# Kernel tuning notes

Hardware: AMD Instinct MI355X
Metric: run time of the kernel (lower is better)

The kernel has to match this reference:

```python
import jax, jax.numpy as jnp
import numpy as np

N = 3072          # num nodes
H = 256           # hidden_features
B = 4             # num_heads
HD = H // B       # per-head dim
PRIOR_MU = 1.0
PRIOR_SIGMA = 1.0
LN_EPS = 1e-5


def setup_inputs() -> dict:
    key = jax.random.key(0)
    ks = jax.random.split(key, 12)
    s = 0.02  # weight init scale
    return {
        "h": jax.random.normal(ks[0], (N, H), jnp.float32),
        "gamma": jnp.ones((H,), jnp.float32),
        "beta": jnp.zeros((H,), jnp.float32),
        "W_k": jax.random.normal(ks[1], (H, H), jnp.float32) * s,
        "b_k": jnp.zeros((H,), jnp.float32),
        "W_mu": jax.random.normal(ks[2], (H, H), jnp.float32) * s,
        "b_mu": jnp.zeros((H,), jnp.float32),
        "W_ls": jax.random.normal(ks[3], (H, H), jnp.float32) * s,
        "b_ls": jnp.zeros((H,), jnp.float32),
        "W_v": jax.random.normal(ks[4], (H * B, H), jnp.float32) * s,
        "b_v": jnp.zeros((H,), jnp.float32),
        "diffusion": jax.random.uniform(ks[5], (N, N, 1), jnp.float32),
        "eps": jax.random.normal(ks[6], (N, N, B), jnp.float32),
    }


def reference(h, gamma, beta, W_k, b_k, W_mu, b_mu, W_ls, b_ls, W_v, b_v, diffusion, eps):
    h0 = h
    # LayerNorm
    mean = jnp.mean(h, axis=-1, keepdims=True)
    var = jnp.var(h, axis=-1, keepdims=True)
    hn = (h - mean) * jax.lax.rsqrt(var + LN_EPS) * gamma + beta
    # Q/K-style projections, split into heads: [N, HD, B]
    k = (hn @ W_k + b_k).reshape(N, HD, B)
    mu = (hn @ W_mu + b_mu).reshape(N, HD, B)
    ls = (hn @ W_ls + b_ls).reshape(N, HD, B)
    scale = HD ** -0.5
    mu = jnp.einsum('xyb,zyb->xzb', k, mu) * scale       # [N, N, B]
    ls = jnp.einsum('xyb,zyb->xzb', k, ls) * scale       # [N, N, B]
    sigma = jax.nn.softplus(ls)
    # KL(LogNormal(mu, sigma) || LogNormal(log(prior_mu), prior_sigma))
    mu_p = jnp.log(jnp.asarray(PRIOR_MU, h.dtype))
    sig_p = jnp.asarray(PRIOR_SIGMA, h.dtype)
    kl = (jnp.log(sig_p / sigma)
          + (sigma ** 2 + (mu - mu_p) ** 2) / (2.0 * sig_p ** 2)
          - 0.5)
    kl = (kl * jnp.sign(diffusion)).sum(-1).mean()
    # reparameterized LogNormal sample, masked by diffusion matrix
    a = jnp.exp(mu + sigma * eps) * diffusion            # [N, N, B]
    # L1 normalize over source-node axis (dim=-2), torch F.normalize semantics
    denom = jnp.clip(jnp.sum(jnp.abs(a), axis=-2, keepdims=True), 1e-12)
    a = a / denom
    # diffusion-weighted aggregation: [N, B, H] -> [N, B*H]
    out = jnp.einsum('xyb,yz->xbz', a, hn).reshape(N, B * H)
    out = out @ W_v + b_v                                 # fc_v (dropout = eval mode)
    out = jax.nn.elu(out) + h0
    return out, kl
```

## Files before the change

### kernel.cpp

```cpp
#include <hip/hip_runtime.h>
#include <hip/hip_bf16.h>


#define NN 3072
#define HH 256
#define NB 4
#define HD 64
constexpr int KMLSZ = 192 * 2 * 64 * 8;

typedef __attribute__((ext_vector_type(8))) short bf16x8;
typedef __attribute__((ext_vector_type(4))) float f32x4;

static __device__ inline short f2bf(float f) {
    __hip_bfloat16 h = __float2bfloat16(f);
    return __builtin_bit_cast(short, h);
}

typedef const __attribute__((address_space(1))) unsigned int* gas_ptr;
typedef __attribute__((address_space(3))) unsigned int* las_ptr;
static __device__ inline void gload_lds16(const void* g, void* l) {
    __builtin_amdgcn_global_load_lds((gas_ptr)g, (las_ptr)l, 16, 0, 0);
}

__global__ void k0_prep(const float* __restrict__ Wk, const float* __restrict__ Wmu,
                        const float* __restrict__ Wls, const float* __restrict__ bk,
                        const float* __restrict__ bmu, const float* __restrict__ bls,
                        const float* __restrict__ Wv, short* __restrict__ WTcat,
                        float* __restrict__ biascat, short* __restrict__ WvT,
                        float* __restrict__ denom) {
    __shared__ float t[64][65];
    int bx = blockIdx.x;
    if (bx < 48) {
        int mat = bx >> 4;
        int by = (bx >> 2) & 3, bc = bx & 3;
        int y0 = by * 64, c0 = bc * 64;
        const float* W = (mat == 0) ? Wk : (mat == 1 ? Wmu : Wls);
        float scale = (mat == 0) ? 0.125f : 1.f;
        int r = threadIdx.x >> 4, c4 = (threadIdx.x & 15) * 4;
#pragma unroll
        for (int i = 0; i < 4; i++) {
            int yl = r + i * 16;
            float4 v = *(const float4*)(W + (y0 + yl) * 256 + c0 + c4);
            t[yl][c4] = v.x; t[yl][c4 + 1] = v.y; t[yl][c4 + 2] = v.z; t[yl][c4 + 3] = v.w;
        }
        __syncthreads();
#pragma unroll
        for (int i = 0; i < 4; i++) {
            int cl = r + i * 16;
            int corig = c0 + cl;
            int cp = mat * 256 + (corig & 3) * 64 + (corig >> 2);
            short4 v = make_short4(f2bf(t[c4][cl] * scale), f2bf(t[c4 + 1][cl] * scale),
                                   f2bf(t[c4 + 2][cl] * scale), f2bf(t[c4 + 3][cl] * scale));
            *(short4*)(WTcat + cp * 256 + y0 + c4) = v;
        }
        return;
    }
    if (bx < 112) {
        int b = bx - 48;
        int bk2 = b >> 2, bn = b & 3;
        int k0 = bk2 * 64, n0 = bn * 64;
        int r = threadIdx.x >> 4, c4 = (threadIdx.x & 15) * 4;
#pragma unroll
        for (int i = 0; i < 4; i++) {
            int kk = r + i * 16;
            float4 v = *(const float4*)(Wv + (k0 + kk) * 256 + n0 + c4);
            t[kk][c4] = v.x; t[kk][c4 + 1] = v.y; t[kk][c4 + 2] = v.z; t[kk][c4 + 3] = v.w;
        }
        __syncthreads();
#pragma unroll
        for (int i = 0; i < 4; i++) {
            int nn = r + i * 16;
            short4 v = make_short4(f2bf(t[c4][nn]), f2bf(t[c4 + 1][nn]),
                                   f2bf(t[c4 + 2][nn]), f2bf(t[c4 + 3][nn]));
            *(short4*)(WvT + (n0 + nn) * 1024 + k0 + c4) = v;
        }
        return;
    }
    if (bx == 112) {
        int cc = threadIdx.x;
        int corig = (cc & 63) * 4 + (cc >> 6);
        biascat[cc] = bk[corig] * 0.125f;
        biascat[256 + cc] = bmu[corig];
        biascat[512 + cc] = bls[corig];
        return;
    }
    int i = (bx - 113) * 256 + threadIdx.x;
    if (i < 13312) denom[i] = 0.f;
}

__global__ void k1_ln(const float* __restrict__ h, const float* __restrict__ gamma,
                      const float* __restrict__ beta, short* __restrict__ hn) {
    int row = blockIdx.x, tid = threadIdx.x;
    float v = h[row * 256 + tid];
    float s = v, s2 = v * v;
    for (int off = 32; off; off >>= 1) {
        s += __shfl_xor(s, off);
        s2 += __shfl_xor(s2, off);
    }
    __shared__ float red[8];
    int w = tid >> 6, lane = tid & 63;
    if (!lane) { red[w] = s; red[4 + w] = s2; }
    __syncthreads();
    s = red[0] + red[1] + red[2] + red[3];
    s2 = red[4] + red[5] + red[6] + red[7];
    float mean = s * (1.f / 256.f);
    float var = s2 * (1.f / 256.f) - mean * mean;
    float rs = rsqrtf(var + 1e-5f);
    hn[row * 256 + tid] = f2bf((v - mean) * rs * gamma[tid] + beta[tid]);
}

__global__ void k1b_tr(const short* __restrict__ hn, short* __restrict__ hnT) {
    __shared__ short t[64][68];
    int bn = blockIdx.x >> 2, bh = blockIdx.x & 3;
    int n0 = bn * 64, h0 = bh * 64;
    int r = threadIdx.x >> 4, c4 = (threadIdx.x & 15) * 4;
#pragma unroll
    for (int i = 0; i < 4; i++) {
        int nn = r + i * 16;
        *(short4*)&t[nn][c4] = *(const short4*)(hn + (n0 + nn) * 256 + h0 + c4);
    }
    __syncthreads();
#pragma unroll
    for (int i = 0; i < 4; i++) {
        int hh = r + i * 16;
        short4 v = make_short4(t[c4][hh], t[c4 + 1][hh], t[c4 + 2][hh], t[c4 + 3][hh]);
        *(short4*)(hnT + (h0 + hh) * NN + n0 + c4) = v;
    }
}

__global__ __launch_bounds__(256) void k2_proj(const short* __restrict__ hn,
                                               const short* __restrict__ WTcat,
                                               const float* __restrict__ biascat,
                                               short* __restrict__ kml) {
    int bx = blockIdx.x;
    int mt = bx / 12, nb = bx % 12;
    int m0 = mt * 64, n0 = nb * 64;
    int tid = threadIdx.x, w = tid >> 6, lane = tid & 63, q = lane >> 4, c = lane & 15;
    int mrow = m0 + w * 16;
    f32x4 acc[4] = {{0, 0, 0, 0}, {0, 0, 0, 0}, {0, 0, 0, 0}, {0, 0, 0, 0}};
    for (int k0 = 0; k0 < 256; k0 += 32) {
        bf16x8 af = *(const bf16x8*)(hn + (mrow + c) * 256 + k0 + q * 8);
#pragma unroll
        for (int nt = 0; nt < 4; nt++) {
            bf16x8 bf = *(const bf16x8*)(WTcat + (n0 + nt * 16 + c) * 256 + k0 + q * 8);
            acc[nt] = __builtin_amdgcn_mfma_f32_16x16x32_bf16(af, bf, acc[nt], 0, 0, 0);
        }
    }
#pragma unroll
    for (int nt = 0; nt < 4; nt++) {
        int cp = n0 + nt * 16 + c;
        float bias = biascat[cp];
        int mat = cp >> 8, b = (cp >> 6) & 3, y = cp & 63;
        short* dst = kml + (size_t)(mat * 4 + b) * KMLSZ;
        int kh2 = y >> 5, lq = (y >> 3) & 3, j = y & 7;
        int zt = mt * 4 + w;
#pragma unroll
        for (int r = 0; r < 4; r++) {
            int ml = 4 * q + r;
            dst[(((zt * 2 + kh2) * 64) + lq * 16 + ml) * 8 + j] = f2bf(acc[nt][r] + bias);
        }
    }
}

__global__ __launch_bounds__(256) void k3a_elem(
    const short* __restrict__ kml, const float* __restrict__ eps,
    const float* __restrict__ diff, short* __restrict__ apk,
    float* __restrict__ denom, float* __restrict__ klsum) {
    __shared__ short frag[2][16][512];
    __shared__ float klred[4];
    const int tid = threadIdx.x;
    const int w = tid >> 6, lane = tid & 63, q = lane >> 4, c = lane & 15;
    const int xb = blockIdx.x % 48;
    const int zc = blockIdx.x / 48;
    const int xt = xb * 4 + w;
    const int x0 = xt * 16;

    auto stage = [&](int buf, int zt2) {
#pragma unroll
        for (int i = 0; i < 4; i++) {
            int f = w * 4 + i;
            int mat = f >> 3, bh = (f >> 1) & 3, kh = f & 1;
            const short* plane = kml + (size_t)((mat + 1) * 4 + bh) * KMLSZ;
            gload_lds16(plane + ((zt2 * 2 + kh) * 64 + lane) * 8, &frag[buf][f][0]);
        }
    };

    bf16x8 qf[NB][2];
#pragma unroll
    for (int b = 0; b < NB; b++)
#pragma unroll
        for (int kh = 0; kh < 2; kh++)
            qf[b][kh] = *(const bf16x8*)(kml + (size_t)b * KMLSZ +
                                         ((xt * 2 + kh) * 64 + lane) * 8);

    stage(0, zc * 4);

    float den_acc[NB] = {0.f, 0.f, 0.f, 0.f};
    float kl_acc = 0.f;
    const size_t xrow = (size_t)(x0 + c) * NN;

    for (int t = 0; t < 4; t++) {
        const int buf = t & 1;
        const int zt2 = zc * 4 + t;
        const int z16 = zt2 * 16;
        __syncthreads();
        if (t < 3) stage(buf ^ 1, zt2 + 1);
        f32x4 e4[4];
        float dif[4];
#pragma unroll
        for (int r = 0; r < 4; r++) {
            e4[r] = *(const f32x4*)(eps + (xrow + (size_t)(z16 + 4 * q + r)) * 4);
            dif[r] = diff[xrow + z16 + 4 * q + r];
        }
#pragma unroll
        for (int b = 0; b < NB; b++) {
            bf16x8 a0 = *(const bf16x8*)&frag[buf][b * 2 + 0][lane * 8];
            bf16x8 a1 = *(const bf16x8*)&frag[buf][b * 2 + 1][lane * 8];
            bf16x8 l0 = *(const bf16x8*)&frag[buf][8 + b * 2 + 0][lane * 8];
            bf16x8 l1 = *(const bf16x8*)&frag[buf][8 + b * 2 + 1][lane * 8];
            f32x4 smu = {0.f, 0.f, 0.f, 0.f};
            smu = __builtin_amdgcn_mfma_f32_16x16x32_bf16(a0, qf[b][0], smu, 0, 0, 0);
            smu = __builtin_amdgcn_mfma_f32_16x16x32_bf16(a1, qf[b][1], smu, 0, 0, 0);
            f32x4 sls = {0.f, 0.f, 0.f, 0.f};
            sls = __builtin_amdgcn_mfma_f32_16x16x32_bf16(l0, qf[b][0], sls, 0, 0, 0);
            sls = __builtin_amdgcn_mfma_f32_16x16x32_bf16(l1, qf[b][1], sls, 0, 0, 0);
            short pk[4];
#pragma unroll
            for (int r = 0; r < 4; r++) {
                float mu = smu[r];
                float ls = sls[r];
                float e = e4[r][b];
                float d = dif[r];
                float ex = __expf(-fabsf(ls));
                float sg = fmaxf(ls, 0.f) + __logf(1.f + ex);
                float kle = -__logf(sg) + 0.5f * (sg * sg + mu * mu) - 0.5f;
                float sgn = (d > 0.f) ? 1.f : ((d < 0.f) ? -1.f : 0.f);
                kl_acc += sgn * kle;
                float av = __expf(mu + sg * e) * d;
                den_acc[b] += fabsf(av);
                pk[r] = f2bf(av);
            }
            *(short4*)(apk + (((size_t)b * 192 + xt) * 192 + zt2) * 256 + c * 16 + q * 4) =
                make_short4(pk[0], pk[1], pk[2], pk[3]);
        }
    }
#pragma unroll
    for (int b = 0; b < NB; b++) {
        float d = den_acc[b];
        d += __shfl_down(d, 32);
        d += __shfl_down(d, 16);
        if (q == 0) atomicAdd(&denom[(x0 + c) * NB + b], d);
    }
    for (int off = 32; off; off >>= 1) kl_acc += __shfl_xor(kl_acc, off);
    if (lane == 0) klred[w] = kl_acc;
    __syncthreads();
    if (tid == 0) atomicAdd(klsum, klred[0] + klred[1] + klred[2] + klred[3]);
}

__global__ __launch_bounds__(256) void k3b_agg(
    const short* __restrict__ apk, const short* __restrict__ hnT,
    const float* __restrict__ denom, short* __restrict__ aggn) {
    __shared__ float red[2][64 * 33];
    const int tid = threadIdx.x;
    const int w = tid >> 6, lane = tid & 63, q = lane >> 4, c = lane & 15;
    const int kw = w >> 1, nw = w & 1;
    const int bid = blockIdx.x;
    const int b = bid & 3;
    const int nb = (bid >> 2) & 3;
    const int mb = bid >> 4;
    const int m0 = mb * 64;
    const int n0 = nb * 64 + nw * 32;
    const int q2 = q >> 1, q1 = q & 1;

    f32x4 acc[4][2];
#pragma unroll
    for (int i = 0; i < 4; i++)
#pragma unroll
        for (int j = 0; j < 2; j++) acc[i][j] = (f32x4){0.f, 0.f, 0.f, 0.f};

    const size_t abase = ((size_t)b * 192 + mb * 4) * 192 * 256;
    for (int ks = 0; ks < 48; ks++) {
        const int kglob = kw * 1536 + ks * 32;
        const int T2 = kw * 96 + ks * 2;
        bf16x8 af[4], bf[2];
#pragma unroll
        for (int mt = 0; mt < 4; mt++)
            af[mt] = *(const bf16x8*)(apk + abase +
                                      (size_t)(mt * 192 + T2 + q2) * 256 + c * 16 + q1 * 8);
#pragma unroll
        for (int nt = 0; nt < 2; nt++)
            bf[nt] = *(const bf16x8*)(hnT + (size_t)(n0 + nt * 16 + c) * NN + kglob + q * 8);
#pragma unroll
        for (int mt = 0; mt < 4; mt++)
#pragma unroll
            for (int nt = 0; nt < 2; nt++)
                acc[mt][nt] = __builtin_amdgcn_mfma_f32_16x16x32_bf16(
                    af[mt], bf[nt], acc[mt][nt], 0, 0, 0);
    }

    if (kw == 1) {
#pragma unroll
        for (int mt = 0; mt < 4; mt++)
#pragma unroll
            for (int nt = 0; nt < 2; nt++)
#pragma unroll
                for (int r = 0; r < 4; r++)
                    red[nw][(mt * 16 + 4 * q + r) * 33 + nt * 16 + c] = acc[mt][nt][r];
    }
    __syncthreads();
    if (kw == 0) {
#pragma unroll
        for (int mt = 0; mt < 4; mt++)
#pragma unroll
            for (int r = 0; r < 4; r++) {
                int x = m0 + mt * 16 + 4 * q + r;
                float rcp = 1.f / fmaxf(denom[x * 4 + b], 1e-12f);
#pragma unroll
                for (int nt = 0; nt < 2; nt++) {
                    float s = acc[mt][nt][r] + red[nw][(mt * 16 + 4 * q + r) * 33 + nt * 16 + c];
                    aggn[(size_t)x * 1024 + b * 256 + n0 + nt * 16 + c] = f2bf(s * rcp);
                }
            }
    }
}

__global__ __launch_bounds__(256) void k4_out(const short* __restrict__ aggn,
                                              const short* __restrict__ WvT,
                                              const float* __restrict__ bv,
                                              const float* __restrict__ h,
                                              const float* __restrict__ klsum,
                                              float* __restrict__ out) {
    int bx = blockIdx.x;
    int mt = bx >> 2, nb = bx & 3;
    int m0 = mt * 64, n0 = nb * 64;
    int tid = threadIdx.x, w = tid >> 6, lane = tid & 63, q = lane >> 4, c = lane & 15;
    int mrow = m0 + w * 16;
    f32x4 acc[4] = {{0, 0, 0, 0}, {0, 0, 0, 0}, {0, 0, 0, 0}, {0, 0, 0, 0}};
    for (int k0 = 0; k0 < 1024; k0 += 32) {
        bf16x8 af = *(const bf16x8*)(aggn + (mrow + c) * 1024 + k0 + q * 8);
#pragma unroll
        for (int nt = 0; nt < 4; nt++) {
            bf16x8 bf = *(const bf16x8*)(WvT + (n0 + nt * 16 + c) * 1024 + k0 + q * 8);
            acc[nt] = __builtin_amdgcn_mfma_f32_16x16x32_bf16(af, bf, acc[nt], 0, 0, 0);
        }
    }
#pragma unroll
    for (int nt = 0; nt < 4; nt++) {
        int col = n0 + nt * 16 + c;
        float bias = bv[col];
#pragma unroll
        for (int r = 0; r < 4; r++) {
            int row = mrow + 4 * q + r;
            float v = acc[nt][r] + bias;
            v = (v > 0.f) ? v : (__expf(v) - 1.f);
            out[row * 256 + col] = v + h[row * 256 + col];
        }
    }
    if (bx == 0 && tid == 0) out[786432] = klsum[0] * (1.0f / 9437184.0f);
}

extern "C" void kernel_launch(void* const* d_in, const int* in_sizes, int n_in,
                              void* d_out, int out_size, void* d_ws, size_t ws_size,
                              hipStream_t stream) {
    const float* h = (const float*)d_in[0];
    const float* gamma = (const float*)d_in[1];
    const float* beta = (const float*)d_in[2];
    const float* Wk = (const float*)d_in[3];
    const float* bk = (const float*)d_in[4];
    const float* Wmu = (const float*)d_in[5];
    const float* bmu = (const float*)d_in[6];
    const float* Wls = (const float*)d_in[7];
    const float* bls = (const float*)d_in[8];
    const float* Wv = (const float*)d_in[9];
    const float* bv = (const float*)d_in[10];
    const float* diff = (const float*)d_in[11];
    const float* eps = (const float*)d_in[12];
    float* out = (float*)d_out;

    char* p = (char*)d_ws;
    short* apk = (short*)p;    p += (size_t)75497472;
    float* denom = (float*)p;  p += 49152;
    float* klsum = (float*)p;  p += 4096;
    short* hn = (short*)p;     p += 1572864;
    short* hnT = (short*)p;    p += 1572864;
    short* kml = (short*)p;    p += 4718592;
    short* WTcat = (short*)p;  p += 393216;
    float* biasc = (float*)p;  p += 4096;
    short* WvT = (short*)p;
    p += 524288;
    short* aggn = (short*)p;

    k0_prep<<<165, 256, 0, stream>>>(Wk, Wmu, Wls, bk, bmu, bls, Wv, WTcat, biasc, WvT,
                                     denom);
    k1_ln<<<3072, 256, 0, stream>>>(h, gamma, beta, hn);
    k1b_tr<<<192, 256, 0, stream>>>(hn, hnT);
    k2_proj<<<576, 256, 0, stream>>>(hn, WTcat, biasc, kml);
    k3a_elem<<<48 * 48, 256, 0, stream>>>(kml, eps, diff, apk, denom, klsum);
    k3b_agg<<<48 * 4 * 4, 256, 0, stream>>>(apk, hnT, denom, aggn);
    k4_out<<<192, 256, 0, stream>>>(aggn, WvT, bv, h, klsum, out);
}
```

Measured before the change: 433.9 us.

## Drop LDS staging of mu/ls fragments, prefetch eps/diff with nontemporal loads

In the elementwise KL/sample kernel, the double-buffered LDS staging of mu/ls projection fragments and its block barriers are removed. Each wave now reads those fragments straight from global memory (a small, cache-resident buffer). The next z-tile's eps and diffusion values are register-prefetched with nontemporal loads, and the packed attention matrix read in the aggregation kernel also uses nontemporal loads. The intent is to remove sync overhead and keep streamed data from polluting cache, at the cost of redundant global/L2 fragment reads across waves and higher register pressure.

```diff
diff --git a/kernel.cpp b/kernel.cpp
--- a/kernel.cpp
+++ b/kernel.cpp
@@ -14,12 +14,6 @@
 static __device__ inline short f2bf(float f) {
     __hip_bfloat16 h = __float2bfloat16(f);
     return __builtin_bit_cast(short, h);
-}
-
-typedef const __attribute__((address_space(1))) unsigned int* gas_ptr;
-typedef __attribute__((address_space(3))) unsigned int* las_ptr;
-static __device__ inline void gload_lds16(const void* g, void* l) {
-    __builtin_amdgcn_global_load_lds((gas_ptr)g, (las_ptr)l, 16, 0, 0);
 }
 
 __global__ void k0_prep(const float* __restrict__ Wk, const float* __restrict__ Wmu,
@@ -166,7 +160,6 @@
     const short* __restrict__ kml, const float* __restrict__ eps,
     const float* __restrict__ diff, short* __restrict__ apk,
     float* __restrict__ denom, float* __restrict__ klsum) {
-    __shared__ short frag[2][16][512];
     __shared__ float klred[4];
     const int tid = threadIdx.x;
     const int w = tid >> 6, lane = tid & 63, q = lane >> 4, c = lane & 15;
@@ -175,16 +168,6 @@
     const int xt = xb * 4 + w;
     const int x0 = xt * 16;
 
-    auto stage = [&](int buf, int zt2) {
-#pragma unroll
-        for (int i = 0; i < 4; i++) {
-            int f = w * 4 + i;
-            int mat = f >> 3, bh = (f >> 1) & 3, kh = f & 1;
-            const short* plane = kml + (size_t)((mat + 1) * 4 + bh) * KMLSZ;
-            gload_lds16(plane + ((zt2 * 2 + kh) * 64 + lane) * 8, &frag[buf][f][0]);
-        }
-    };
-
     bf16x8 qf[NB][2];
 #pragma unroll
     for (int b = 0; b < NB; b++)
@@ -193,31 +176,46 @@
             qf[b][kh] = *(const bf16x8*)(kml + (size_t)b * KMLSZ +
                                          ((xt * 2 + kh) * 64 + lane) * 8);
 
-    stage(0, zc * 4);
-
     float den_acc[NB] = {0.f, 0.f, 0.f, 0.f};
     float kl_acc = 0.f;
     const size_t xrow = (size_t)(x0 + c) * NN;
 
+    f32x4 e_nxt[4];
+    float d_nxt[4];
+    {
+        const int z16 = zc * 64;
+#pragma unroll
+        for (int r = 0; r < 4; r++) {
+            e_nxt[r] = __builtin_nontemporal_load(
+                (const f32x4*)(eps + (xrow + (size_t)(z16 + 4 * q + r)) * 4));
+            d_nxt[r] = __builtin_nontemporal_load(diff + xrow + z16 + 4 * q + r);
+        }
+    }
+
+#pragma unroll
     for (int t = 0; t < 4; t++) {
-        const int buf = t & 1;
         const int zt2 = zc * 4 + t;
-        const int z16 = zt2 * 16;
-        __syncthreads();
-        if (t < 3) stage(buf ^ 1, zt2 + 1);
         f32x4 e4[4];
         float dif[4];
 #pragma unroll
-        for (int r = 0; r < 4; r++) {
-            e4[r] = *(const f32x4*)(eps + (xrow + (size_t)(z16 + 4 * q + r)) * 4);
-            dif[r] = diff[xrow + z16 + 4 * q + r];
+        for (int r = 0; r < 4; r++) { e4[r] = e_nxt[r]; dif[r] = d_nxt[r]; }
+        if (t < 3) {
+            const int z16 = (zt2 + 1) * 16;
+#pragma unroll
+            for (int r = 0; r < 4; r++) {
+                e_nxt[r] = __builtin_nontemporal_load(
+                    (const f32x4*)(eps + (xrow + (size_t)(z16 + 4 * q + r)) * 4));
+                d_nxt[r] = __builtin_nontemporal_load(diff + xrow + z16 + 4 * q + r);
+            }
         }
 #pragma unroll
         for (int b = 0; b < NB; b++) {
-            bf16x8 a0 = *(const bf16x8*)&frag[buf][b * 2 + 0][lane * 8];
-            bf16x8 a1 = *(const bf16x8*)&frag[buf][b * 2 + 1][lane * 8];
-            bf16x8 l0 = *(const bf16x8*)&frag[buf][8 + b * 2 + 0][lane * 8];
-            bf16x8 l1 = *(const bf16x8*)&frag[buf][8 + b * 2 + 1][lane * 8];
+            const short* mup = kml + (size_t)(NB + b) * KMLSZ;
+            const short* lsp = kml + (size_t)(2 * NB + b) * KMLSZ;
+            bf16x8 a0 = *(const bf16x8*)(mup + ((zt2 * 2 + 0) * 64 + lane) * 8);
+            bf16x8 a1 = *(const bf16x8*)(mup + ((zt2 * 2 + 1) * 64 + lane) * 8);
+            bf16x8 l0 = *(const bf16x8*)(lsp + ((zt2 * 2 + 0) * 64 + lane) * 8);
+            bf16x8 l1 = *(const bf16x8*)(lsp + ((zt2 * 2 + 1) * 64 + lane) * 8);
             f32x4 smu = {0.f, 0.f, 0.f, 0.f};
             smu = __builtin_amdgcn_mfma_f32_16x16x32_bf16(a0, qf[b][0], smu, 0, 0, 0);
             smu = __builtin_amdgcn_mfma_f32_16x16x32_bf16(a1, qf[b][1], smu, 0, 0, 0);
@@ -285,8 +283,9 @@
         bf16x8 af[4], bf[2];
 #pragma unroll
         for (int mt = 0; mt < 4; mt++)
-            af[mt] = *(const bf16x8*)(apk + abase +
-                                      (size_t)(mt * 192 + T2 + q2) * 256 + c * 16 + q1 * 8);
+            af[mt] = __builtin_nontemporal_load(
+                (const bf16x8*)(apk + abase + (size_t)(mt * 192 + T2 + q2) * 256 +
+                                c * 16 + q1 * 8));
 #pragma unroll
         for (int nt = 0; nt < 2; nt++)
             bf[nt] = *(const bf16x8*)(hnT + (size_t)(n0 + nt * 16 + c) * NN + kglob + q * 8);
@@ -386,8 +385,7 @@
     short* kml = (short*)p;    p += 4718592;
     short* WTcat = (short*)p;  p += 393216;
     float* biasc = (float*)p;  p += 4096;
-    short* WvT = (short*)p;
-    p += 524288;
+    short* WvT = (short*)p;    p += 524288;
     short* aggn = (short*)p;
 
     k0_prep<<<165, 256, 0, stream>>>(Wk, Wmu, Wls, bk, bmu, bls, Wv, WTcat, biasc, WvT,
```

Result: slower. 463.9 us (+6.9%).
